# Optimization experiments

Hardware: AMD Instinct MI355X
Metric: run time of the kernel (lower is better)

Reference implementation:

```python
import jax, jax.numpy as jnp
import numpy as np

C = 128  # n_filters; input channels must equal n_filters due to residual


def setup_inputs() -> dict:
    key = jax.random.key(0)
    kx, kw = jax.random.split(key)
    x = jax.random.normal(kx, (8, 64, 512, C), dtype=jnp.float32)
    # 1x1 conv, no bias == dense over channel axis: [C, 2C]
    W_qkv = jax.random.normal(kw, (C, 2 * C), dtype=jnp.float32) * (1.0 / np.sqrt(C))
    return {"x": x, "W_qkv": W_qkv}


def reference(x, W_qkv):
    # qkv: [B,H,W,2C]; split -> qk [B,H,W,C] -> q,k [B,H,W,C/2]; v [B,H,W,C]
    qkv = jnp.einsum('bhwc,cd->bhwd', x, W_qkv)
    half = C // 2
    q = qkv[..., :half]
    k = qkv[..., half:C]
    v = qkv[..., C:]
    # scores over the W (time) axis; NOTE: original applies no 1/sqrt(d) scaling
    scores = jnp.einsum('bhqc,bhkc->bhqk', q, k)  # [B,H,W,W]
    w = jax.nn.softmax(scores, axis=-1)
    y = jnp.einsum('bhqk,bhkc->bhqc', w, v)  # [B,H,W,C]
    y = x + y  # with_skip_connection=True
    return (y, w)
```

## Files before the change

### kernel.cpp

```cpp
#include <hip/hip_runtime.h>
#include <hip/hip_bf16.h>

typedef short s16x8 __attribute__((ext_vector_type(8)));
typedef float f32x4 __attribute__((ext_vector_type(4)));

#define MFMA_BF16(a,b,c) __builtin_amdgcn_mfma_f32_16x16x32_bf16((a),(b),(c),0,0,0)

static __device__ __forceinline__ unsigned short f2bf(float f){
  unsigned u = __builtin_bit_cast(unsigned, f);
  u += 0x7fffu + ((u >> 16) & 1u);
  return (unsigned short)(u >> 16);
}
static __device__ __forceinline__ float bf2f(unsigned short h){
  unsigned u = ((unsigned)h) << 16;
  return __builtin_bit_cast(float, u);
}
static __device__ __forceinline__ int swz128(int row, int col){
  return row*128 + ((col & 7) | (((col >> 3) ^ (row & 7)) << 3));
}
static __device__ __forceinline__ int swz64(int row, int col){
  return row*64 + ((col & 7) | (((col >> 3) ^ (row & 7)) << 3));
}
static __device__ __forceinline__ int swz512(int row, int col){
  return row*512 + ((col & 7) | (((col >> 3) ^ (row & 7)) << 3));
}

__global__ __launch_bounds__(256) void k0_wt(const float* __restrict__ W,
                                             unsigned short* __restrict__ wtH,
                                             unsigned short* __restrict__ wtL){
  __shared__ float tile[32][257];
  const int t = threadIdx.x;
  for (int cc = 0; cc < 128; cc += 32){
    #pragma unroll
    for (int k = 0; k < 32; ++k)
      tile[k][t] = W[(size_t)(cc + k)*256 + t];
    __syncthreads();
    #pragma unroll
    for (int k = 0; k < 32; ++k){
      const float v = tile[k][t];
      const int c = cc + k;
      const unsigned short h = f2bf(v);
      const unsigned short l = f2bf(v - bf2f(h));
      const int cs = (c & 7) | (((c >> 3) ^ (t & 7)) << 3);
      wtH[t*128 + cs] = h;
      wtL[t*128 + cs] = l;
    }
    __syncthreads();
  }
}

__global__ __launch_bounds__(512,2) void k1_qkv(const float* __restrict__ x,
    const unsigned short* __restrict__ wtH, const unsigned short* __restrict__ wtL,
    float* __restrict__ qk, unsigned short* __restrict__ vT){
  __shared__ unsigned short xh[16384], xl[16384], wth[16384], wtl[16384];
  const int t = threadIdx.x;
  const int lane = t & 63, wid = t >> 6;
  const int li = lane & 15, g = lane >> 4;
  const int m0 = blockIdx.x * 128;
  const int wm = wid >> 2, wn = wid & 3;

  {
    const int row = t >> 2, cb = (t & 3) * 32;
    const float* src = x + (size_t)(m0 + row)*128 + cb;
    #pragma unroll
    for (int gg = 0; gg < 4; ++gg){
      const float4 v0 = ((const float4*)src)[2*gg];
      const float4 v1 = ((const float4*)src)[2*gg + 1];
      const float vv[8] = {v0.x,v0.y,v0.z,v0.w,v1.x,v1.y,v1.z,v1.w};
      s16x8 h, l;
      #pragma unroll
      for (int j = 0; j < 8; ++j){
        const unsigned short hb = f2bf(vv[j]);
        h[j] = (short)hb;
        l[j] = (short)f2bf(vv[j] - bf2f(hb));
      }
      const int idx = swz128(row, cb + 8*gg);
      *(s16x8*)&xh[idx] = h;
      *(s16x8*)&xl[idx] = l;
    }
  }

  for (int nh = 0; nh < 2; ++nh){
    if (nh) __syncthreads();
    {
      const s16x8* sh = (const s16x8*)(wtH + nh*16384);
      const s16x8* sl = (const s16x8*)(wtL + nh*16384);
      #pragma unroll
      for (int i2 = 0; i2 < 4; ++i2){
        ((s16x8*)wth)[t + i2*512] = sh[t + i2*512];
        ((s16x8*)wtl)[t + i2*512] = sl[t + i2*512];
      }
    }
    __syncthreads();

    f32x4 acc[4][2] = {};
    #pragma unroll
    for (int ks = 0; ks < 4; ++ks){
      const int col = ks*32 + g*8;
      s16x8 ah[4], al[4], bh[2], bl[2];
      #pragma unroll
      for (int mi = 0; mi < 4; ++mi){
        const int idx = swz128(wm*64 + mi*16 + li, col);
        ah[mi] = *(const s16x8*)&xh[idx];
        al[mi] = *(const s16x8*)&xl[idx];
      }
      #pragma unroll
      for (int ni = 0; ni < 2; ++ni){
        const int idx = swz128(wn*32 + ni*16 + li, col);
        bh[ni] = *(const s16x8*)&wth[idx];
        bl[ni] = *(const s16x8*)&wtl[idx];
      }
      #pragma unroll
      for (int mi = 0; mi < 4; ++mi)
        #pragma unroll
        for (int ni = 0; ni < 2; ++ni){
          acc[mi][ni] = MFMA_BF16(ah[mi], bh[ni], acc[mi][ni]);
          acc[mi][ni] = MFMA_BF16(ah[mi], bl[ni], acc[mi][ni]);
          acc[mi][ni] = MFMA_BF16(al[mi], bh[ni], acc[mi][ni]);
        }
    }

    if (nh == 0){
      #pragma unroll
      for (int mi = 0; mi < 4; ++mi)
        #pragma unroll
        for (int ni = 0; ni < 2; ++ni)
          #pragma unroll
          for (int r = 0; r < 4; ++r){
            const int grow = m0 + wm*64 + mi*16 + g*4 + r;
            const int coln = wn*32 + ni*16 + li;
            qk[(size_t)grow*128 + coln] = acc[mi][ni][r];
          }
    } else {
      #pragma unroll
      for (int mi = 0; mi < 4; ++mi)
        #pragma unroll
        for (int ni = 0; ni < 2; ++ni)
          #pragma unroll
          for (int r = 0; r < 4; ++r){
            const int grow = m0 + wm*64 + mi*16 + g*4 + r;
            const int ch = wn*32 + ni*16 + li;
            const int head = grow >> 9, pos = grow & 511;
            vT[((size_t)head << 16) + ch*512 + pos] = f2bf(acc[mi][ni][r]);
          }
    }
  }
}

__global__ __launch_bounds__(512,2) void k2_attn(const float* __restrict__ qk,
    const unsigned short* __restrict__ vT, const float* __restrict__ x,
    float* __restrict__ y, float* __restrict__ wout){
  __shared__ unsigned short qh[4096], ql[4096];
  __shared__ unsigned short wlds[32768];
  __shared__ float redm[512], reds[512];

  const int t = threadIdx.x;
  const int lane = t & 63, wid = t >> 6;
  const int li = lane & 15, g = lane >> 4;
  const int bi = blockIdx.x;
  const int head = (bi & 7) + 8*(bi >> 6);
  const int qt = (bi >> 3) & 7;
  const size_t hbase = (size_t)head * 512;
  const int q0 = qt * 64;

  {
    const int row = t >> 3, c8 = (t & 7) * 8;
    const float* src = qk + (hbase + q0 + row)*128 + c8;
    const float4 v0 = ((const float4*)src)[0];
    const float4 v1 = ((const float4*)src)[1];
    const float vv[8] = {v0.x,v0.y,v0.z,v0.w,v1.x,v1.y,v1.z,v1.w};
    s16x8 h, l;
    #pragma unroll
    for (int j = 0; j < 8; ++j){
      const unsigned short hb = f2bf(vv[j]);
      h[j] = (short)hb;
      l[j] = (short)f2bf(vv[j] - bf2f(hb));
    }
    const int idx = swz64(row, c8);
    *(s16x8*)&qh[idx] = h;
    *(s16x8*)&ql[idx] = l;
  }
  __syncthreads();

  const int kbase = wid * 64;
  f32x4 acc[4][4] = {};
  #pragma unroll
  for (int ks = 0; ks < 2; ++ks){
    s16x8 kh[4], kl[4];
    #pragma unroll
    for (int ni = 0; ni < 4; ++ni){
      const float* kp = qk + (hbase + kbase + ni*16 + li)*128 + 64 + ks*32 + g*8;
      const float4 a = ((const float4*)kp)[0];
      const float4 b = ((const float4*)kp)[1];
      const float vv[8] = {a.x,a.y,a.z,a.w,b.x,b.y,b.z,b.w};
      #pragma unroll
      for (int j = 0; j < 8; ++j){
        const unsigned short hb = f2bf(vv[j]);
        kh[ni][j] = (short)hb;
        kl[ni][j] = (short)f2bf(vv[j] - bf2f(hb));
      }
    }
    const int col = ks*32 + g*8;
    s16x8 ah[4], al[4];
    #pragma unroll
    for (int mi = 0; mi < 4; ++mi){
      const int idx = swz64(mi*16 + li, col);
      ah[mi] = *(const s16x8*)&qh[idx];
      al[mi] = *(const s16x8*)&ql[idx];
    }
    #pragma unroll
    for (int mi = 0; mi < 4; ++mi)
      #pragma unroll
      for (int ni = 0; ni < 4; ++ni){
        acc[mi][ni] = MFMA_BF16(ah[mi], kh[ni], acc[mi][ni]);
        acc[mi][ni] = MFMA_BF16(ah[mi], kl[ni], acc[mi][ni]);
        acc[mi][ni] = MFMA_BF16(al[mi], kh[ni], acc[mi][ni]);
      }
  }

  #pragma unroll
  for (int mi = 0; mi < 4; ++mi)
    #pragma unroll
    for (int r = 0; r < 4; ++r){
      float m = fmaxf(fmaxf(acc[mi][0][r], acc[mi][1][r]),
                      fmaxf(acc[mi][2][r], acc[mi][3][r]));
      #pragma unroll
      for (int d = 1; d < 16; d <<= 1) m = fmaxf(m, __shfl_xor(m, d));
      if (li == 0) redm[(mi*16 + g*4 + r)*8 + wid] = m;
    }
  __syncthreads();
  float inv[4][4];
  #pragma unroll
  for (int mi = 0; mi < 4; ++mi)
    #pragma unroll
    for (int r = 0; r < 4; ++r){
      const int row = mi*16 + g*4 + r;
      float m = redm[row*8];
      #pragma unroll
      for (int kk = 1; kk < 8; ++kk) m = fmaxf(m, redm[row*8 + kk]);
      float s = 0.f;
      #pragma unroll
      for (int ni = 0; ni < 4; ++ni){
        const float e = __expf(acc[mi][ni][r] - m);
        acc[mi][ni][r] = e;
        s += e;
      }
      #pragma unroll
      for (int d = 1; d < 16; d <<= 1) s += __shfl_xor(s, d);
      if (li == 0) reds[row*8 + wid] = s;
    }
  __syncthreads();
  #pragma unroll
  for (int mi = 0; mi < 4; ++mi)
    #pragma unroll
    for (int r = 0; r < 4; ++r){
      const int row = mi*16 + g*4 + r;
      float s = reds[row*8];
      #pragma unroll
      for (int kk = 1; kk < 8; ++kk) s += reds[row*8 + kk];
      inv[mi][r] = 1.0f / s;
    }

  #pragma unroll
  for (int mi = 0; mi < 4; ++mi)
    #pragma unroll
    for (int ni = 0; ni < 4; ++ni)
      #pragma unroll
      for (int r = 0; r < 4; ++r){
        const int row = mi*16 + g*4 + r;
        const int col = kbase + ni*16 + li;
        const float wv = acc[mi][ni][r] * inv[mi][r];
        wout[(hbase + q0 + row)*512 + col] = wv;
        wlds[swz512(row, col)] = f2bf(wv);
      }
  __syncthreads();

  const int c0 = wid * 16;
  f32x4 yacc[4] = {};
  const unsigned short* vhead = vT + ((size_t)head << 16) + (size_t)(c0 + li)*512;
  #pragma unroll
  for (int kt = 0; kt < 16; ++kt){
    const int kp0 = kt*32 + g*8;
    const s16x8 vb = *(const s16x8*)&vhead[kp0];
    #pragma unroll
    for (int mi = 0; mi < 4; ++mi){
      const s16x8 aw = *(const s16x8*)&wlds[swz512(mi*16 + li, kp0)];
      yacc[mi] = MFMA_BF16(aw, vb, yacc[mi]);
    }
  }

  #pragma unroll
  for (int mi = 0; mi < 4; ++mi)
    #pragma unroll
    for (int r = 0; r < 4; ++r){
      const int row = mi*16 + g*4 + r;
      const size_t idx = (hbase + q0 + row)*128 + c0 + li;
      y[idx] = x[idx] + yacc[mi][r];
    }
}

extern "C" void kernel_launch(void* const* d_in, const int* in_sizes, int n_in,
                              void* d_out, int out_size, void* d_ws, size_t ws_size,
                              hipStream_t stream){
  (void)in_sizes; (void)n_in; (void)out_size; (void)ws_size;
  const float* x = (const float*)d_in[0];
  const float* W = (const float*)d_in[1];
  float* y    = (float*)d_out;
  float* wout = y + (size_t)33554432;

  char* ws = (char*)d_ws;
  float*          qk  = (float*)ws;
  unsigned short* vT  = (unsigned short*)(ws + 134217728ull);
  unsigned short* wtH = (unsigned short*)(ws + 201326592ull);
  unsigned short* wtL = (unsigned short*)(ws + 201392128ull);

  hipLaunchKernelGGL(k0_wt,   dim3(1),    dim3(256), 0, stream, W, wtH, wtL);
  hipLaunchKernelGGL(k1_qkv,  dim3(2048), dim3(512), 0, stream, x, wtH, wtL, qk, vT);
  hipLaunchKernelGGL(k2_attn, dim3(4096), dim3(512), 0, stream, qk, vT, x, y, wout);
}
```

Measured before the change: 539.8 us.

## Precompute bf16 hi/lo Q and K in QKV kernel, read fragments directly from global

```diff
diff --git a/kernel.cpp b/kernel.cpp
--- a/kernel.cpp
+++ b/kernel.cpp
@@ -15,44 +15,28 @@
   unsigned u = ((unsigned)h) << 16;
   return __builtin_bit_cast(float, u);
 }
-static __device__ __forceinline__ int swz128(int row, int col){
-  return row*128 + ((col & 7) | (((col >> 3) ^ (row & 7)) << 3));
-}
-static __device__ __forceinline__ int swz64(int row, int col){
-  return row*64 + ((col & 7) | (((col >> 3) ^ (row & 7)) << 3));
-}
-static __device__ __forceinline__ int swz512(int row, int col){
-  return row*512 + ((col & 7) | (((col >> 3) ^ (row & 7)) << 3));
-}
-
-__global__ __launch_bounds__(256) void k0_wt(const float* __restrict__ W,
+static __device__ __forceinline__ int swzi(int row, int col, int lw){
+  const int chunk = (col >> 3) ^ ((row ^ (row >> 3)) & 7);
+  return row*lw + (chunk << 3) + (col & 7);
+}
+
+__global__ __launch_bounds__(128) void k0_wt(const float* __restrict__ W,
                                              unsigned short* __restrict__ wtH,
                                              unsigned short* __restrict__ wtL){
-  __shared__ float tile[32][257];
-  const int t = threadIdx.x;
-  for (int cc = 0; cc < 128; cc += 32){
-    #pragma unroll
-    for (int k = 0; k < 32; ++k)
-      tile[k][t] = W[(size_t)(cc + k)*256 + t];
-    __syncthreads();
-    #pragma unroll
-    for (int k = 0; k < 32; ++k){
-      const float v = tile[k][t];
-      const int c = cc + k;
-      const unsigned short h = f2bf(v);
-      const unsigned short l = f2bf(v - bf2f(h));
-      const int cs = (c & 7) | (((c >> 3) ^ (t & 7)) << 3);
-      wtH[t*128 + cs] = h;
-      wtL[t*128 + cs] = l;
-    }
-    __syncthreads();
-  }
-}
-
-__global__ __launch_bounds__(512,2) void k1_qkv(const float* __restrict__ x,
+  const int n = blockIdx.x;
+  const int c = threadIdx.x;
+  const float v = W[(size_t)c*256 + n];
+  const unsigned short h = f2bf(v);
+  wtH[n*128 + c] = h;
+  wtL[n*128 + c] = f2bf(v - bf2f(h));
+}
+
+__global__ __launch_bounds__(512,4) void k1_qkv(const float* __restrict__ x,
     const unsigned short* __restrict__ wtH, const unsigned short* __restrict__ wtL,
-    float* __restrict__ qk, unsigned short* __restrict__ vT){
-  __shared__ unsigned short xh[16384], xl[16384], wth[16384], wtl[16384];
+    unsigned short* __restrict__ qh, unsigned short* __restrict__ ql,
+    unsigned short* __restrict__ kh, unsigned short* __restrict__ kl,
+    unsigned short* __restrict__ vT){
+  __shared__ unsigned short xh[16384], xl[16384];
   const int t = threadIdx.x;
   const int lane = t & 63, wid = t >> 6;
   const int li = lane & 15, g = lane >> 4;
@@ -74,50 +58,37 @@
         h[j] = (short)hb;
         l[j] = (short)f2bf(vv[j] - bf2f(hb));
       }
-      const int idx = swz128(row, cb + 8*gg);
+      const int idx = swzi(row, cb + 8*gg, 128);
       *(s16x8*)&xh[idx] = h;
       *(s16x8*)&xl[idx] = l;
     }
   }
+  __syncthreads();
 
   for (int nh = 0; nh < 2; ++nh){
-    if (nh) __syncthreads();
-    {
-      const s16x8* sh = (const s16x8*)(wtH + nh*16384);
-      const s16x8* sl = (const s16x8*)(wtL + nh*16384);
-      #pragma unroll
-      for (int i2 = 0; i2 < 4; ++i2){
-        ((s16x8*)wth)[t + i2*512] = sh[t + i2*512];
-        ((s16x8*)wtl)[t + i2*512] = sl[t + i2*512];
-      }
-    }
-    __syncthreads();
-
     f32x4 acc[4][2] = {};
     #pragma unroll
     for (int ks = 0; ks < 4; ++ks){
       const int col = ks*32 + g*8;
-      s16x8 ah[4], al[4], bh[2], bl[2];
+      s16x8 ah[4], al[4];
       #pragma unroll
       for (int mi = 0; mi < 4; ++mi){
-        const int idx = swz128(wm*64 + mi*16 + li, col);
+        const int idx = swzi(wm*64 + mi*16 + li, col, 128);
         ah[mi] = *(const s16x8*)&xh[idx];
         al[mi] = *(const s16x8*)&xl[idx];
       }
       #pragma unroll
       for (int ni = 0; ni < 2; ++ni){
-        const int idx = swz128(wn*32 + ni*16 + li, col);
-        bh[ni] = *(const s16x8*)&wth[idx];
-        bl[ni] = *(const s16x8*)&wtl[idx];
-      }
-      #pragma unroll
-      for (int mi = 0; mi < 4; ++mi)
+        const size_t boff = (size_t)(nh*128 + wn*32 + ni*16 + li)*128 + col;
+        const s16x8 bh = *(const s16x8*)(wtH + boff);
+        const s16x8 bl = *(const s16x8*)(wtL + boff);
         #pragma unroll
-        for (int ni = 0; ni < 2; ++ni){
-          acc[mi][ni] = MFMA_BF16(ah[mi], bh[ni], acc[mi][ni]);
-          acc[mi][ni] = MFMA_BF16(ah[mi], bl[ni], acc[mi][ni]);
-          acc[mi][ni] = MFMA_BF16(al[mi], bh[ni], acc[mi][ni]);
+        for (int mi = 0; mi < 4; ++mi){
+          acc[mi][ni] = MFMA_BF16(ah[mi], bh, acc[mi][ni]);
+          acc[mi][ni] = MFMA_BF16(ah[mi], bl, acc[mi][ni]);
+          acc[mi][ni] = MFMA_BF16(al[mi], bh, acc[mi][ni]);
         }
+      }
     }
 
     if (nh == 0){
@@ -129,7 +100,12 @@
           for (int r = 0; r < 4; ++r){
             const int grow = m0 + wm*64 + mi*16 + g*4 + r;
             const int coln = wn*32 + ni*16 + li;
-            qk[(size_t)grow*128 + coln] = acc[mi][ni][r];
+            const float v = acc[mi][ni][r];
+            const unsigned short h = f2bf(v);
+            const unsigned short lo = f2bf(v - bf2f(h));
+            const size_t off = (size_t)grow*64 + (coln & 63);
+            if (wn < 2){ qh[off] = h; ql[off] = lo; }
+            else       { kh[off] = h; kl[off] = lo; }
           }
     } else {
       #pragma unroll
@@ -147,10 +123,11 @@
   }
 }
 
-__global__ __launch_bounds__(512,2) void k2_attn(const float* __restrict__ qk,
+__global__ __launch_bounds__(512,4) void k2_attn(
+    const unsigned short* __restrict__ qh, const unsigned short* __restrict__ ql,
+    const unsigned short* __restrict__ kh, const unsigned short* __restrict__ kl,
     const unsigned short* __restrict__ vT, const float* __restrict__ x,
     float* __restrict__ y, float* __restrict__ wout){
-  __shared__ unsigned short qh[4096], ql[4096];
   __shared__ unsigned short wlds[32768];
   __shared__ float redm[512], reds[512];
 
@@ -162,60 +139,31 @@
   const int qt = (bi >> 3) & 7;
   const size_t hbase = (size_t)head * 512;
   const int q0 = qt * 64;
-
-  {
-    const int row = t >> 3, c8 = (t & 7) * 8;
-    const float* src = qk + (hbase + q0 + row)*128 + c8;
-    const float4 v0 = ((const float4*)src)[0];
-    const float4 v1 = ((const float4*)src)[1];
-    const float vv[8] = {v0.x,v0.y,v0.z,v0.w,v1.x,v1.y,v1.z,v1.w};
-    s16x8 h, l;
-    #pragma unroll
-    for (int j = 0; j < 8; ++j){
-      const unsigned short hb = f2bf(vv[j]);
-      h[j] = (short)hb;
-      l[j] = (short)f2bf(vv[j] - bf2f(hb));
-    }
-    const int idx = swz64(row, c8);
-    *(s16x8*)&qh[idx] = h;
-    *(s16x8*)&ql[idx] = l;
-  }
-  __syncthreads();
-
   const int kbase = wid * 64;
+
   f32x4 acc[4][4] = {};
   #pragma unroll
   for (int ks = 0; ks < 2; ++ks){
-    s16x8 kh[4], kl[4];
-    #pragma unroll
-    for (int ni = 0; ni < 4; ++ni){
-      const float* kp = qk + (hbase + kbase + ni*16 + li)*128 + 64 + ks*32 + g*8;
-      const float4 a = ((const float4*)kp)[0];
-      const float4 b = ((const float4*)kp)[1];
-      const float vv[8] = {a.x,a.y,a.z,a.w,b.x,b.y,b.z,b.w};
-      #pragma unroll
-      for (int j = 0; j < 8; ++j){
-        const unsigned short hb = f2bf(vv[j]);
-        kh[ni][j] = (short)hb;
-        kl[ni][j] = (short)f2bf(vv[j] - bf2f(hb));
-      }
-    }
     const int col = ks*32 + g*8;
     s16x8 ah[4], al[4];
     #pragma unroll
     for (int mi = 0; mi < 4; ++mi){
-      const int idx = swz64(mi*16 + li, col);
-      ah[mi] = *(const s16x8*)&qh[idx];
-      al[mi] = *(const s16x8*)&ql[idx];
-    }
-    #pragma unroll
-    for (int mi = 0; mi < 4; ++mi)
-      #pragma unroll
-      for (int ni = 0; ni < 4; ++ni){
-        acc[mi][ni] = MFMA_BF16(ah[mi], kh[ni], acc[mi][ni]);
-        acc[mi][ni] = MFMA_BF16(ah[mi], kl[ni], acc[mi][ni]);
-        acc[mi][ni] = MFMA_BF16(al[mi], kh[ni], acc[mi][ni]);
-      }
+      const size_t aoff = (hbase + q0 + mi*16 + li)*64 + col;
+      ah[mi] = *(const s16x8*)(qh + aoff);
+      al[mi] = *(const s16x8*)(ql + aoff);
+    }
+    #pragma unroll
+    for (int ni = 0; ni < 4; ++ni){
+      const size_t boff = (hbase + kbase + ni*16 + li)*64 + col;
+      const s16x8 bh = *(const s16x8*)(kh + boff);
+      const s16x8 bl = *(const s16x8*)(kl + boff);
+      #pragma unroll
+      for (int mi = 0; mi < 4; ++mi){
+        acc[mi][ni] = MFMA_BF16(ah[mi], bh, acc[mi][ni]);
+        acc[mi][ni] = MFMA_BF16(ah[mi], bl, acc[mi][ni]);
+        acc[mi][ni] = MFMA_BF16(al[mi], bh, acc[mi][ni]);
+      }
+    }
   }
 
   #pragma unroll
@@ -270,8 +218,8 @@
         const int row = mi*16 + g*4 + r;
         const int col = kbase + ni*16 + li;
         const float wv = acc[mi][ni][r] * inv[mi][r];
-        wout[(hbase + q0 + row)*512 + col] = wv;
-        wlds[swz512(row, col)] = f2bf(wv);
+        __builtin_nontemporal_store(wv, &wout[(hbase + q0 + row)*512 + col]);
+        wlds[swzi(row, col, 512)] = f2bf(wv);
       }
   __syncthreads();
 
@@ -284,7 +232,7 @@
     const s16x8 vb = *(const s16x8*)&vhead[kp0];
     #pragma unroll
     for (int mi = 0; mi < 4; ++mi){
-      const s16x8 aw = *(const s16x8*)&wlds[swz512(mi*16 + li, kp0)];
+      const s16x8 aw = *(const s16x8*)&wlds[swzi(mi*16 + li, kp0, 512)];
       yacc[mi] = MFMA_BF16(aw, vb, yacc[mi]);
     }
   }
@@ -295,7 +243,7 @@
     for (int r = 0; r < 4; ++r){
       const int row = mi*16 + g*4 + r;
       const size_t idx = (hbase + q0 + row)*128 + c0 + li;
-      y[idx] = x[idx] + yacc[mi][r];
+      __builtin_nontemporal_store(x[idx] + yacc[mi][r], &y[idx]);
     }
 }
 
@@ -309,12 +257,17 @@
   float* wout = y + (size_t)33554432;
 
   char* ws = (char*)d_ws;
-  float*          qk  = (float*)ws;
+  unsigned short* qh  = (unsigned short*)(ws);
+  unsigned short* ql  = (unsigned short*)(ws +  33554432ull);
+  unsigned short* kh  = (unsigned short*)(ws +  67108864ull);
+  unsigned short* kl  = (unsigned short*)(ws + 100663296ull);
   unsigned short* vT  = (unsigned short*)(ws + 134217728ull);
   unsigned short* wtH = (unsigned short*)(ws + 201326592ull);
   unsigned short* wtL = (unsigned short*)(ws + 201392128ull);
 
-  hipLaunchKernelGGL(k0_wt,   dim3(1),    dim3(256), 0, stream, W, wtH, wtL);
-  hipLaunchKernelGGL(k1_qkv,  dim3(2048), dim3(512), 0, stream, x, wtH, wtL, qk, vT);
-  hipLaunchKernelGGL(k2_attn, dim3(4096), dim3(512), 0, stream, qk, vT, x, y, wout);
-}
+  hipLaunchKernelGGL(k0_wt,   dim3(256),  dim3(128), 0, stream, W, wtH, wtL);
+  hipLaunchKernelGGL(k1_qkv,  dim3(2048), dim3(512), 0, stream, x, wtH, wtL,
+                     qh, ql, kh, kl, vT);
+  hipLaunchKernelGGL(k2_attn, dim3(4096), dim3(512), 0, stream,
+                     qh, ql, kh, kl, vT, x, y, wout);
+}
```

After: 671.1 us. +24.3%, slower.
